# Optimization experiments

Hardware: AMD Instinct MI355X
Metric: run time of the kernel (lower is better)

Reference implementation:

```python
import jax, jax.numpy as jnp
import numpy as np

B, S, D, H = 8, 1024, 1024, 32


def setup_inputs() -> dict:
    key = jax.random.key(0)
    ks = jax.random.split(key, 32)
    w = lambda k, shape: jax.random.normal(k, shape, jnp.float32) * 0.02
    inp = {
        "poi_emb": jax.random.normal(ks[0], (B, S, D), jnp.float32),
        "svi_emb": jax.random.normal(ks[1], (B, S, D), jnp.float32),
        "poly_emb": jax.random.normal(ks[2], (B, S, D), jnp.float32),
        # shared multi-head attention (one module reused for all 4 calls)
        "Wq": w(ks[3], (D, D)), "bq": w(ks[4], (D,)),
        "Wk": w(ks[5], (D, D)), "bk": w(ks[6], (D,)),
        "Wv": w(ks[7], (D, D)), "bv": w(ks[8], (D,)),
        "Wo": w(ks[9], (D, D)), "bo": w(ks[10], (D,)),
        # poi_trans / svi_trans / poly_trans: Linear -> ReLU -> LayerNorm
        "Wpoi": w(ks[11], (D, D)), "bpoi": w(ks[12], (D,)),
        "gpoi": jnp.ones((D,), jnp.float32), "betapoi": jnp.zeros((D,), jnp.float32),
        "Wsvi": w(ks[13], (D, D)), "bsvi": w(ks[14], (D,)),
        "gsvi": jnp.ones((D,), jnp.float32), "betasvi": jnp.zeros((D,), jnp.float32),
        "Wpoly": w(ks[15], (D, D)), "bpoly": w(ks[16], (D,)),
        "gpoly": jnp.ones((D,), jnp.float32), "betapoly": jnp.zeros((D,), jnp.float32),
        # gate (Linear(2D,D)+sigmoid), filtration_gate (Linear(2D,D)+relu), out_trans (Linear(D,D))
        "Wg": w(ks[17], (2 * D, D)), "bg": w(ks[18], (D,)),
        "Wf": w(ks[19], (2 * D, D)), "bf": w(ks[20], (D,)),
        "Wt": w(ks[21], (D, D)), "bt": w(ks[22], (D,)),
    }
    return inp


def _ln(x, g, b, eps=1e-5):
    m = x.mean(-1, keepdims=True)
    v = ((x - m) ** 2).mean(-1, keepdims=True)
    return (x - m) / jnp.sqrt(v + eps) * g + b


def _trans(x, W, b, g, be):
    return _ln(jax.nn.relu(x @ W + b), g, be)


def _mha(q, k, v, Wq, bq, Wk, bk, Wv, bv, Wo, bo):
    Bn, Sq, Dm = q.shape
    dk = Dm // H
    Q = (q @ Wq + bq).reshape(Bn, Sq, H, dk)
    K = (k @ Wk + bk).reshape(Bn, -1, H, dk)
    V = (v @ Wv + bv).reshape(Bn, -1, H, dk)
    scores = jnp.einsum('bqhd,bkhd->bhqk', Q, K) / jnp.sqrt(jnp.float32(dk))
    attn = jax.nn.softmax(scores, axis=-1)
    out = jnp.einsum('bhqk,bkhd->bqhd', attn, V).reshape(Bn, Sq, Dm)
    return out @ Wo + bo


def reference(poi_emb, svi_emb, poly_emb, Wq, bq, Wk, bk, Wv, bv, Wo, bo,
              Wpoi, bpoi, gpoi, betapoi, Wsvi, bsvi, gsvi, betasvi,
              Wpoly, bpoly, gpoly, betapoly, Wg, bg, Wf, bf, Wt, bt):
    mha = lambda q, k, v: _mha(q, k, v, Wq, bq, Wk, bk, Wv, bv, Wo, bo)

    poi = _trans(poi_emb, Wpoi, bpoi, gpoi, betapoi)
    svi = _trans(svi_emb, Wsvi, bsvi, gsvi, betasvi)
    svi_feat = mha(svi, poi, poi)
    poi_feat = mha(poi, svi_feat, svi_feat)
    poi_feat = poi_feat + poi
    svi_feat = svi_feat + svi
    gate = jax.nn.sigmoid(jnp.concatenate([poi_feat, svi_feat], -1) @ Wg + bg)
    svi_fusion = gate * poi_feat + (1.0 - gate) * svi_feat
    filt = jax.nn.relu(jnp.concatenate([poi_feat, svi_fusion], -1) @ Wf + bf)
    out = filt @ Wt + bt

    # num == 3 branch
    poly = _trans(poly_emb, Wpoly, bpoly, gpoly, betapoly)
    poi2 = out
    poly_feat = mha(poly, poi2, poi2)
    poi_feat2 = mha(poi2, poly_feat, poly_feat)
    poly_feat = poly_feat + poly
    poi_feat2 = poi_feat2 + poi2
    gate2 = jax.nn.sigmoid(jnp.concatenate([poi_feat2, poly_feat], -1) @ Wg + bg)
    poly_fusion = gate2 * poi_feat2 + (1.0 - gate2) * poly_feat
    filt2 = jax.nn.relu(jnp.concatenate([poi_feat2, poly_fusion], -1) @ Wf + bf)
    return filt2 @ Wt + bt
```

## Files before the change

### kernel.cpp

```cpp
#include <hip/hip_runtime.h>
#include <hip/hip_bf16.h>


typedef unsigned short u16;
typedef __bf16 bf16x8_t __attribute__((ext_vector_type(8)));
typedef float f32x4 __attribute__((ext_vector_type(4)));

__device__ __forceinline__ u16 f2bf(float f) {
  union { __hip_bfloat16 h; u16 u; } c; c.h = __float2bfloat16(f); return c.u;
}
__device__ __forceinline__ float bf2f(u16 u) {
  union { unsigned v; float f; } c; c.v = ((unsigned)u) << 16; return c.f;
}

__device__ __forceinline__ void gl16(const void* g, void* l) {
  __builtin_amdgcn_global_load_lds((const __attribute__((address_space(1))) unsigned*)g,
                                   (__attribute__((address_space(3))) unsigned*)l, 16, 0, 0);
}

__global__ void fill_kernel(float4* o, float v) {
  int i = blockIdx.x * 256 + threadIdx.x;
  float4 x = {v, v, v, v};
  o[i] = x;
}

struct Conv3 { const float4* s[3]; ushort4* d[3]; };
__global__ void conv3_kernel(Conv3 p) {
  int seg = blockIdx.x >> 13;
  int i = (blockIdx.x & 8191) * 256 + threadIdx.x;
  float4 v = p.s[seg][i];
  ushort4 o; o.x = f2bf(v.x); o.y = f2bf(v.y); o.z = f2bf(v.z); o.w = f2bf(v.w);
  p.d[seg][i] = o;
}

struct WPack { const float* s[8]; u16* d[8]; };
__global__ void transpose_w_kernel(WPack p, int K) {
  const float* W = p.s[blockIdx.z];
  u16* Wt = p.d[blockIdx.z];
  __shared__ float tile[32][33];
  int tx = threadIdx.x, ty = threadIdx.y;
  int n0 = blockIdx.x * 32, k0 = blockIdx.y * 32;
#pragma unroll
  for (int i = 0; i < 4; i++)
    tile[ty + 8 * i][tx] = W[(size_t)(k0 + ty + 8 * i) * 1024 + n0 + tx];
  __syncthreads();
#pragma unroll
  for (int i = 0; i < 4; i++)
    Wt[(size_t)(n0 + ty + 8 * i) * K + k0 + tx] = f2bf(tile[tx][ty + 8 * i]);
}

struct GemmSeg {
  const u16 *A, *A2, *Bt;
  const float *bias, *bias1, *resF;
  float* outF; u16 *outH0, *outH1;
  const u16 *fx, *fy;
  int K, act, nctl, blk0;
  float oscale;
};
struct GemmArgs { GemmSeg s[3]; int nseg; int nwg8; };

__global__ __launch_bounds__(256) void gemm_mega(GemmArgs ga) {
  int orig = blockIdx.x;
  int bid = (orig & 7) * ga.nwg8 + (orig >> 3);
  int si = 0;
  if (ga.nseg > 1 && bid >= ga.s[1].blk0) si = 1;
  if (ga.nseg > 2 && bid >= ga.s[2].blk0) si = 2;
  GemmSeg sg = ga.s[si];
  int lb = bid - sg.blk0;
  int nct = 1 << sg.nctl;
  int bx = lb & (nct - 1), by = lb >> sg.nctl;

  __shared__ __align__(16) u16 lA[128 * 64];
  __shared__ __align__(16) u16 lB[128 * 64];
  int tid = threadIdx.x, lane = tid & 63, w = tid >> 6;
  int g = lane >> 4, li = lane & 15;
  int row0 = by * 128, col0 = bx * 128;
  int wr = (w >> 1) * 64, wc = (w & 1) * 64;
  f32x4 acc[4][4] = {};

  for (int k0 = 0; k0 < sg.K; k0 += 64) {
    const u16* Abase = (k0 < 1024) ? sg.A : sg.A2;
    int ka = k0 & 1023;
#pragma unroll
    for (int i = 0; i < 4; i++) {
      int c = tid + i * 256; int r = c >> 3, kc = c & 7;
      gl16(Abase + (size_t)(row0 + r) * 1024 + ka + kc * 8, lA + c * 8);
    }
#pragma unroll
    for (int i = 0; i < 4; i++) {
      int c = tid + i * 256; int n = c >> 3, kc = c & 7;
      gl16(sg.Bt + (size_t)(col0 + n) * sg.K + k0 + kc * 8, lB + c * 8);
    }
    __syncthreads();
#pragma unroll
    for (int kk = 0; kk < 2; kk++) {
      bf16x8_t af[4], bfr[4];
#pragma unroll
      for (int mr = 0; mr < 4; mr++)
        af[mr] = *(const bf16x8_t*)(lA + (wr + mr * 16 + li) * 64 + kk * 32 + g * 8);
#pragma unroll
      for (int nr = 0; nr < 4; nr++)
        bfr[nr] = *(const bf16x8_t*)(lB + (wc + nr * 16 + li) * 64 + kk * 32 + g * 8);
#pragma unroll
      for (int mr = 0; mr < 4; mr++)
#pragma unroll
        for (int nr = 0; nr < 4; nr++)
          acc[mr][nr] = __builtin_amdgcn_mfma_f32_16x16x32_bf16(af[mr], bfr[nr], acc[mr][nr], 0, 0, 0);
    }
    __syncthreads();
  }

#pragma unroll
  for (int nr = 0; nr < 4; nr++) {
    int col = col0 + wc + nr * 16 + li;
    int hi = col >> 10, colm = col & 1023;
    float bv = (hi ? sg.bias1 : sg.bias)[colm];
    u16* oh = hi ? sg.outH1 : sg.outH0;
#pragma unroll
    for (int mr = 0; mr < 4; mr++) {
      int rowb = row0 + wr + mr * 16 + g * 4;
#pragma unroll
      for (int r = 0; r < 4; r++) {
        size_t off = (size_t)(rowb + r) * 1024 + colm;
        float v = acc[mr][nr][r] + bv;
        if (sg.resF) v += sg.resF[off];
        if (sg.act == 1) v = fmaxf(v, 0.f);
        else if (sg.act == 2) {
          v = 1.f / (1.f + __expf(-v));
          if (sg.fx) v = v * bf2f(sg.fx[off]) + (1.f - v) * bf2f(sg.fy[off]);
        }
        v *= sg.oscale;
        if (sg.outF) sg.outF[off] = v;
        if (oh) oh[off] = f2bf(v);
      }
    }
  }
}

struct LnSeg { const u16* in; const float* ga; const float* be; float* outF; u16* outH; };
struct LnArgs { LnSeg s[3]; };
__global__ __launch_bounds__(256) void ln3_kernel(LnArgs la) {
  int seg = blockIdx.x >> 13;
  int row = blockIdx.x & 8191;
  LnSeg sg = la.s[seg];
  int t = threadIdx.x, lane = t & 63, w = t >> 6;
  ushort4 xi = ((const ushort4*)(sg.in + (size_t)row * 1024))[t];
  float4 x;
  x.x = fmaxf(bf2f(xi.x), 0.f); x.y = fmaxf(bf2f(xi.y), 0.f);
  x.z = fmaxf(bf2f(xi.z), 0.f); x.w = fmaxf(bf2f(xi.w), 0.f);
  float s1 = x.x + x.y + x.z + x.w;
  float s2 = x.x * x.x + x.y * x.y + x.z * x.z + x.w * x.w;
#pragma unroll
  for (int m = 1; m < 64; m <<= 1) { s1 += __shfl_xor(s1, m); s2 += __shfl_xor(s2, m); }
  __shared__ float red[8];
  if (lane == 0) { red[w] = s1; red[4 + w] = s2; }
  __syncthreads();
  s1 = red[0] + red[1] + red[2] + red[3];
  s2 = red[4] + red[5] + red[6] + red[7];
  float mean = s1 * (1.f / 1024.f);
  float var = s2 * (1.f / 1024.f) - mean * mean;
  float rstd = rsqrtf(var + 1e-5f);
  float4 gg = ((const float4*)sg.ga)[t], bb = ((const float4*)sg.be)[t];
  float4 y;
  y.x = (x.x - mean) * rstd * gg.x + bb.x;
  y.y = (x.y - mean) * rstd * gg.y + bb.y;
  y.z = (x.z - mean) * rstd * gg.z + bb.z;
  y.w = (x.w - mean) * rstd * gg.w + bb.w;
  if (sg.outF) ((float4*)(sg.outF + (size_t)row * 1024))[t] = y;
  ushort4 h; h.x = f2bf(y.x); h.y = f2bf(y.y); h.z = f2bf(y.z); h.w = f2bf(y.w);
  ((ushort4*)(sg.outH + (size_t)row * 1024))[t] = h;
}

__global__ void add2_kernel(const ushort4* __restrict__ a, const ushort4* __restrict__ b,
                            ushort4* __restrict__ o) {
  int i = blockIdx.x * 256 + threadIdx.x;
  ushort4 x = a[i], y = b[i];
  ushort4 h;
  h.x = f2bf(bf2f(x.x) + bf2f(y.x)); h.y = f2bf(bf2f(x.y) + bf2f(y.y));
  h.z = f2bf(bf2f(x.z) + bf2f(y.z)); h.w = f2bf(bf2f(x.w) + bf2f(y.w));
  o[i] = h;
}

__global__ __launch_bounds__(256) void attn_kernel(
    const u16* __restrict__ Q, const u16* __restrict__ Kb,
    const u16* __restrict__ Vb, u16* __restrict__ O) {
  int orig = blockIdx.x;
  int bid = (orig & 7) * 512 + (orig >> 3);
  int qt = bid & 15, h = (bid >> 4) & 31, b = bid >> 9;
  int tid = threadIdx.x, lane = tid & 63, w = tid >> 6;
  int g = lane >> 4, li = lane & 15;
  __shared__ __align__(16) u16 lK[128 * 40];
  __shared__ __align__(16) u16 lV[32 * 152];
  __shared__ __align__(16) u16 lP[4][16 * 152];
  int q0 = qt * 64 + w * 16;

  bf16x8_t aq = *(const bf16x8_t*)(Q + ((size_t)(b * 1024 + q0 + li) << 10) + h * 32 + g * 8);
  const f32x4 fzero = {0.f, 0.f, 0.f, 0.f};
  f32x4 oacc[2] = {};
  float mrun[4], lrun[4];
#pragma unroll
  for (int r = 0; r < 4; r++) { mrun[r] = -1e30f; lrun[r] = 0.f; }

  for (int kt = 0; kt < 1024; kt += 128) {
    __syncthreads();
#pragma unroll
    for (int i = 0; i < 2; i++) {
      int c2 = tid + i * 256; int key = c2 >> 2, ch = c2 & 3;
      uint4 v = *(const uint4*)(Kb + ((size_t)(b * 1024 + kt + key) << 10) + h * 32 + ch * 8);
      *(uint4*)(lK + key * 40 + ch * 8) = v;
    }
    {
      int p = tid >> 2, ch = tid & 3;
      const u16* vb0 = Vb + ((size_t)(b * 1024 + kt + 2 * p) << 10) + h * 32 + ch * 8;
      uint4 a = *(const uint4*)(vb0);
      uint4 bb = *(const uint4*)(vb0 + 1024);
      unsigned* lv32 = (unsigned*)lV;
#pragma unroll
      for (int j = 0; j < 4; j++) {
        unsigned ax = ((const unsigned*)&a)[j], bx = ((const unsigned*)&bb)[j];
        lv32[(8 * ch + 2 * j) * 76 + p]     = (ax & 0xffffu) | (bx << 16);
        lv32[(8 * ch + 2 * j + 1) * 76 + p] = (ax >> 16) | (bx & 0xffff0000u);
      }
    }
    __syncthreads();

    f32x4 s[8];
#pragma unroll
    for (int sub = 0; sub < 8; sub++) {
      bf16x8_t bk = *(const bf16x8_t*)(lK + (sub * 16 + li) * 40 + g * 8);
      s[sub] = __builtin_amdgcn_mfma_f32_16x16x32_bf16(aq, bk, fzero, 0, 0, 0);
    }
    float mx[4];
#pragma unroll
    for (int r = 0; r < 4; r++) mx[r] = -1e30f;
#pragma unroll
    for (int sub = 0; sub < 8; sub++)
#pragma unroll
      for (int r = 0; r < 4; r++) mx[r] = fmaxf(mx[r], s[sub][r]);
#pragma unroll
    for (int m = 1; m < 16; m <<= 1)
#pragma unroll
      for (int r = 0; r < 4; r++) mx[r] = fmaxf(mx[r], __shfl_xor(mx[r], m));
    bool keep = (mx[0] <= mrun[0] + 8.f) && (mx[1] <= mrun[1] + 8.f) &&
                (mx[2] <= mrun[2] + 8.f) && (mx[3] <= mrun[3] + 8.f);
    if (!__all(keep)) {
#pragma unroll
      for (int r = 0; r < 4; r++) {
        float mn = fmaxf(mrun[r], mx[r]);
        float corr = exp2f(mrun[r] - mn);
        mrun[r] = mn; lrun[r] *= corr;
        oacc[0][r] *= corr; oacc[1][r] *= corr;
      }
    }
    float rs[4] = {0.f, 0.f, 0.f, 0.f};
#pragma unroll
    for (int sub = 0; sub < 8; sub++)
#pragma unroll
      for (int r = 0; r < 4; r++) {
        float p = exp2f(s[sub][r] - mrun[r]);
        s[sub][r] = p; rs[r] += p;
      }
#pragma unroll
    for (int m = 1; m < 16; m <<= 1)
#pragma unroll
      for (int r = 0; r < 4; r++) rs[r] += __shfl_xor(rs[r], m);
#pragma unroll
    for (int r = 0; r < 4; r++) lrun[r] += rs[r];
#pragma unroll
    for (int sub = 0; sub < 8; sub++)
#pragma unroll
      for (int r = 0; r < 4; r++)
        lP[w][(g * 4 + r) * 152 + sub * 16 + li] = f2bf(s[sub][r]);
#pragma unroll
    for (int ks = 0; ks < 4; ks++) {
      bf16x8_t ap = *(const bf16x8_t*)(lP[w] + li * 152 + ks * 32 + g * 8);
#pragma unroll
      for (int nt = 0; nt < 2; nt++) {
        bf16x8_t bv = *(const bf16x8_t*)(lV + (nt * 16 + li) * 152 + ks * 32 + g * 8);
        oacc[nt] = __builtin_amdgcn_mfma_f32_16x16x32_bf16(ap, bv, oacc[nt], 0, 0, 0);
      }
    }
  }
#pragma unroll
  for (int r = 0; r < 4; r++) {
    float inv = 1.f / lrun[r];
#pragma unroll
    for (int nt = 0; nt < 2; nt++)
      O[((size_t)(b * 1024 + q0 + g * 4 + r) << 10) + h * 32 + nt * 16 + li] =
          f2bf(oacc[nt][r] * inv);
  }
}

static GemmSeg mk(const u16* A, const u16* A2, const u16* Bt,
                  const float* bias, const float* bias1, const float* resF,
                  float* outF, u16* oh0, u16* oh1, const u16* fx, const u16* fy,
                  int K, int act, int nctl, float osc) {
  GemmSeg s; s.A = A; s.A2 = A2; s.Bt = Bt; s.bias = bias; s.bias1 = bias1;
  s.resF = resF; s.outF = outF; s.outH0 = oh0; s.outH1 = oh1; s.fx = fx; s.fy = fy;
  s.K = K; s.act = act; s.nctl = nctl; s.blk0 = 0; s.oscale = osc;
  return s;
}

extern "C" void kernel_launch(void* const* d_in, const int* in_sizes, int n_in,
                              void* d_out, int out_size, void* d_ws, size_t ws_size,
                              hipStream_t stream) {
  const float* poi_emb = (const float*)d_in[0];
  const float* svi_emb = (const float*)d_in[1];
  const float* poly_emb = (const float*)d_in[2];
  const float *Wq = (const float*)d_in[3], *bq = (const float*)d_in[4];
  const float *Wk = (const float*)d_in[5], *bk = (const float*)d_in[6];
  const float *Wv = (const float*)d_in[7], *bv = (const float*)d_in[8];
  const float *Wo = (const float*)d_in[9], *bo = (const float*)d_in[10];
  const float *Wpoi = (const float*)d_in[11], *bpoi = (const float*)d_in[12];
  const float *gpoi = (const float*)d_in[13], *betapoi = (const float*)d_in[14];
  const float *Wsvi = (const float*)d_in[15], *bsvi = (const float*)d_in[16];
  const float *gsvi = (const float*)d_in[17], *betasvi = (const float*)d_in[18];
  const float *Wpoly = (const float*)d_in[19], *bpoly = (const float*)d_in[20];
  const float *gpoly = (const float*)d_in[21], *betapoly = (const float*)d_in[22];
  const float *Wg = (const float*)d_in[23], *bg = (const float*)d_in[24];
  const float *Wf = (const float*)d_in[25], *bfilt = (const float*)d_in[26];
  const float *Wt = (const float*)d_in[27], *bt = (const float*)d_in[28];

  const size_t MB = 1u << 20;
  if (ws_size < 168 * MB) {
    fill_kernel<<<out_size / 1024, 256, 0, stream>>>((float4*)d_out, 1e4f);
    return;
  }
  char* ws = (char*)d_ws;
  u16* WqT = (u16*)(ws + 0 * MB);    u16* WkT = (u16*)(ws + 2 * MB);
  u16* WvT = (u16*)(ws + 4 * MB);    u16* WoT = (u16*)(ws + 6 * MB);
  u16* WpoiT = (u16*)(ws + 8 * MB);  u16* WsviT = (u16*)(ws + 10 * MB);
  u16* WpolyT = (u16*)(ws + 12 * MB); u16* WtT = (u16*)(ws + 14 * MB);
  u16* WgT = (u16*)(ws + 16 * MB);   u16* WfT = (u16*)(ws + 20 * MB);
  u16* S0 = (u16*)(ws + 24 * MB);  u16* S1 = (u16*)(ws + 40 * MB);
  u16* S2 = (u16*)(ws + 56 * MB);  u16* S3 = (u16*)(ws + 72 * MB);
  u16* S4 = (u16*)(ws + 88 * MB);  u16* S5 = (u16*)(ws + 104 * MB);
  u16* S6 = (u16*)(ws + 120 * MB);
  float* F = (float*)(ws + 136 * MB);

  const float QS = 0.25503489f;

  WPack p8;
  p8.s[0]=Wq; p8.s[1]=Wk; p8.s[2]=Wv; p8.s[3]=Wo; p8.s[4]=Wpoi; p8.s[5]=Wsvi; p8.s[6]=Wpoly; p8.s[7]=Wt;
  p8.d[0]=WqT; p8.d[1]=WkT; p8.d[2]=WvT; p8.d[3]=WoT; p8.d[4]=WpoiT; p8.d[5]=WsviT; p8.d[6]=WpolyT; p8.d[7]=WtT;
  transpose_w_kernel<<<dim3(32, 32, 8), dim3(32, 8), 0, stream>>>(p8, 1024);
  WPack p2;
  p2.s[0]=Wg; p2.s[1]=Wf; p2.d[0]=WgT; p2.d[1]=WfT;
  for (int i = 2; i < 8; i++) { p2.s[i] = Wg; p2.d[i] = WgT; }
  transpose_w_kernel<<<dim3(32, 64, 2), dim3(32, 8), 0, stream>>>(p2, 2048);

  auto run1 = [&](GemmSeg a) {
    GemmArgs ga; ga.s[0] = a; ga.s[0].blk0 = 0; ga.nseg = 1;
    int nb = 64 << a.nctl; ga.nwg8 = nb / 8;
    gemm_mega<<<nb, 256, 0, stream>>>(ga);
  };
  auto run2 = [&](GemmSeg a, GemmSeg b) {
    GemmArgs ga; ga.s[0] = a; ga.s[1] = b;
    ga.s[0].blk0 = 0; ga.s[1].blk0 = 64 << a.nctl; ga.nseg = 2;
    int nb = (64 << a.nctl) + (64 << b.nctl); ga.nwg8 = nb / 8;
    gemm_mega<<<nb, 256, 0, stream>>>(ga);
  };
  auto run3 = [&](GemmSeg a, GemmSeg b, GemmSeg c) {
    GemmArgs ga; ga.s[0] = a; ga.s[1] = b; ga.s[2] = c;
    ga.s[0].blk0 = 0; ga.s[1].blk0 = 64 << a.nctl;
    ga.s[2].blk0 = ga.s[1].blk0 + (64 << b.nctl); ga.nseg = 3;
    int nb = ga.s[2].blk0 + (64 << c.nctl); ga.nwg8 = nb / 8;
    gemm_mega<<<nb, 256, 0, stream>>>(ga);
  };
  auto attn = [&](const u16* q, const u16* k, const u16* v, u16* o) {
    attn_kernel<<<4096, 256, 0, stream>>>(q, k, v, o);
  };
  auto add2 = [&](const u16* a, const u16* b, u16* o) {
    add2_kernel<<<8192, 256, 0, stream>>>((const ushort4*)a, (const ushort4*)b, (ushort4*)o);
  };

  Conv3 c3;
  c3.s[0] = (const float4*)poi_emb; c3.d[0] = (ushort4*)S0;
  c3.s[1] = (const float4*)svi_emb; c3.d[1] = (ushort4*)S1;
  c3.s[2] = (const float4*)poly_emb; c3.d[2] = (ushort4*)S2;
  conv3_kernel<<<24576, 256, 0, stream>>>(c3);

  run3(mk(S0, 0, WpoiT, bpoi, 0, 0, 0, S3, 0, 0, 0, 1024, 0, 3, 1.f),
       mk(S1, 0, WsviT, bsvi, 0, 0, 0, S4, 0, 0, 0, 1024, 0, 3, 1.f),
       mk(S2, 0, WpolyT, bpoly, 0, 0, 0, S5, 0, 0, 0, 1024, 0, 3, 1.f));
  LnArgs la;
  la.s[0] = LnSeg{S3, gpoi, betapoi, F, S3};
  la.s[1] = LnSeg{S4, gsvi, betasvi, 0, S4};
  la.s[2] = LnSeg{S5, gpoly, betapoly, 0, S5};
  ln3_kernel<<<24576, 256, 0, stream>>>(la);

  run2(mk(S4, 0, WqT, bq, 0, 0, 0, S0, 0, 0, 0, 1024, 0, 3, QS),
       mk(S3, 0, WkT, bk, bv, 0, 0, S1, S2, 0, 0, 1024, 0, 4, 1.f));
  attn(S0, S1, S2, S6);
  run2(mk(S6, 0, WoT, bo, 0, 0, 0, S0, 0, 0, 0, 1024, 0, 3, 1.f),
       mk(S3, 0, WqT, bq, 0, 0, 0, S1, 0, 0, 0, 1024, 0, 3, QS));
  run1(mk(S0, 0, WkT, bk, bv, 0, 0, S2, S6, 0, 0, 1024, 0, 4, 1.f));
  attn(S1, S2, S6, S3);
  run1(mk(S3, 0, WoT, bo, 0, F, 0, S1, 0, 0, 0, 1024, 0, 3, 1.f));
  add2(S0, S4, S4);
  run1(mk(S1, S4, WgT, bg, 0, 0, 0, S0, 0, S1, S4, 2048, 2, 3, 1.f));
  run1(mk(S1, S0, WfT, bfilt, 0, 0, 0, S2, 0, 0, 0, 2048, 1, 3, 1.f));
  run1(mk(S2, 0, WtT, bt, 0, 0, F, S6, 0, 0, 0, 1024, 0, 3, 1.f));

  run2(mk(S5, 0, WqT, bq, 0, 0, 0, S0, 0, 0, 0, 1024, 0, 3, QS),
       mk(S6, 0, WkT, bk, bv, 0, 0, S1, S2, 0, 0, 1024, 0, 4, 1.f));
  attn(S0, S1, S2, S3);
  run2(mk(S3, 0, WoT, bo, 0, 0, 0, S0, 0, 0, 0, 1024, 0, 3, 1.f),
       mk(S6, 0, WqT, bq, 0, 0, 0, S1, 0, 0, 0, 1024, 0, 3, QS));
  run1(mk(S0, 0, WkT, bk, bv, 0, 0, S2, S3, 0, 0, 1024, 0, 4, 1.f));
  attn(S1, S2, S3, S4);
  run1(mk(S4, 0, WoT, bo, 0, F, 0, S1, 0, 0, 0, 1024, 0, 3, 1.f));
  add2(S0, S5, S5);
  run1(mk(S1, S5, WgT, bg, 0, 0, 0, S0, 0, S1, S5, 2048, 2, 3, 1.f));
  run1(mk(S1, S0, WfT, bfilt, 0, 0, 0, S2, 0, 0, 0, 2048, 1, 3, 1.f));
  run1(mk(S2, 0, WtT, bt, 0, 0, (float*)d_out, 0, 0, 0, 0, 1024, 0, 3, 1.f));
}
```

Baseline: 1.825 ms.

## Restructure attention with register K loads, double-buffered V, MFMA row sums; add 64-row GEMM tiles

```diff
diff --git a/kernel.cpp b/kernel.cpp
--- a/kernel.cpp
+++ b/kernel.cpp
@@ -59,7 +59,9 @@
 };
 struct GemmArgs { GemmSeg s[3]; int nseg; int nwg8; };
 
+template <int BM>
 __global__ __launch_bounds__(256) void gemm_mega(GemmArgs ga) {
+  constexpr int MR = BM / 32;
   int orig = blockIdx.x;
   int bid = (orig & 7) * ga.nwg8 + (orig >> 3);
   int si = 0;
@@ -70,19 +72,19 @@
   int nct = 1 << sg.nctl;
   int bx = lb & (nct - 1), by = lb >> sg.nctl;
 
-  __shared__ __align__(16) u16 lA[128 * 64];
+  __shared__ __align__(16) u16 lA[BM * 64];
   __shared__ __align__(16) u16 lB[128 * 64];
   int tid = threadIdx.x, lane = tid & 63, w = tid >> 6;
   int g = lane >> 4, li = lane & 15;
-  int row0 = by * 128, col0 = bx * 128;
-  int wr = (w >> 1) * 64, wc = (w & 1) * 64;
-  f32x4 acc[4][4] = {};
+  int row0 = by * BM, col0 = bx * 128;
+  int wr = (w >> 1) * (BM / 2), wc = (w & 1) * 64;
+  f32x4 acc[MR][4] = {};
 
   for (int k0 = 0; k0 < sg.K; k0 += 64) {
     const u16* Abase = (k0 < 1024) ? sg.A : sg.A2;
     int ka = k0 & 1023;
 #pragma unroll
-    for (int i = 0; i < 4; i++) {
+    for (int i = 0; i < MR; i++) {
       int c = tid + i * 256; int r = c >> 3, kc = c & 7;
       gl16(Abase + (size_t)(row0 + r) * 1024 + ka + kc * 8, lA + c * 8);
     }
@@ -94,15 +96,15 @@
     __syncthreads();
 #pragma unroll
     for (int kk = 0; kk < 2; kk++) {
-      bf16x8_t af[4], bfr[4];
-#pragma unroll
-      for (int mr = 0; mr < 4; mr++)
+      bf16x8_t af[MR], bfr[4];
+#pragma unroll
+      for (int mr = 0; mr < MR; mr++)
         af[mr] = *(const bf16x8_t*)(lA + (wr + mr * 16 + li) * 64 + kk * 32 + g * 8);
 #pragma unroll
       for (int nr = 0; nr < 4; nr++)
         bfr[nr] = *(const bf16x8_t*)(lB + (wc + nr * 16 + li) * 64 + kk * 32 + g * 8);
 #pragma unroll
-      for (int mr = 0; mr < 4; mr++)
+      for (int mr = 0; mr < MR; mr++)
 #pragma unroll
         for (int nr = 0; nr < 4; nr++)
           acc[mr][nr] = __builtin_amdgcn_mfma_f32_16x16x32_bf16(af[mr], bfr[nr], acc[mr][nr], 0, 0, 0);
@@ -117,7 +119,7 @@
     float bv = (hi ? sg.bias1 : sg.bias)[colm];
     u16* oh = hi ? sg.outH1 : sg.outH0;
 #pragma unroll
-    for (int mr = 0; mr < 4; mr++) {
+    for (int mr = 0; mr < MR; mr++) {
       int rowb = row0 + wr + mr * 16 + g * 4;
 #pragma unroll
       for (int r = 0; r < 4; r++) {
@@ -189,101 +191,119 @@
   int qt = bid & 15, h = (bid >> 4) & 31, b = bid >> 9;
   int tid = threadIdx.x, lane = tid & 63, w = tid >> 6;
   int g = lane >> 4, li = lane & 15;
-  __shared__ __align__(16) u16 lK[128 * 40];
-  __shared__ __align__(16) u16 lV[32 * 152];
-  __shared__ __align__(16) u16 lP[4][16 * 152];
+  __shared__ __align__(16) u16 lV[(2 * 32 + 16) * 136];
+  __shared__ __align__(16) u16 lP[4][16 * 136];
   int q0 = qt * 64 + w * 16;
 
+  for (int i = tid; i < 16 * 136; i += 256) {
+    int rr = i / 136;
+    lV[8704 + i] = (rr == 0) ? (u16)0x3f80 : (u16)0;
+  }
+
   bf16x8_t aq = *(const bf16x8_t*)(Q + ((size_t)(b * 1024 + q0 + li) << 10) + h * 32 + g * 8);
+  const u16* kbase = Kb + ((size_t)(b * 1024 + li) << 10) + h * 32 + g * 8;
+  const u16* vb0 = Vb + ((size_t)(b * 1024 + 2 * lane) << 10) + h * 32 + w * 8;
+
   const f32x4 fzero = {0.f, 0.f, 0.f, 0.f};
-  f32x4 oacc[2] = {};
-  float mrun[4], lrun[4];
-#pragma unroll
-  for (int r = 0; r < 4; r++) { mrun[r] = -1e30f; lrun[r] = 0.f; }
-
-  for (int kt = 0; kt < 1024; kt += 128) {
-    __syncthreads();
-#pragma unroll
-    for (int i = 0; i < 2; i++) {
-      int c2 = tid + i * 256; int key = c2 >> 2, ch = c2 & 3;
-      uint4 v = *(const uint4*)(Kb + ((size_t)(b * 1024 + kt + key) << 10) + h * 32 + ch * 8);
-      *(uint4*)(lK + key * 40 + ch * 8) = v;
-    }
-    {
-      int p = tid >> 2, ch = tid & 3;
-      const u16* vb0 = Vb + ((size_t)(b * 1024 + kt + 2 * p) << 10) + h * 32 + ch * 8;
-      uint4 a = *(const uint4*)(vb0);
-      uint4 bb = *(const uint4*)(vb0 + 1024);
-      unsigned* lv32 = (unsigned*)lV;
+  f32x4 oacc[2] = {}; f32x4 osum = {};
+  float mrun[4];
+#pragma unroll
+  for (int r = 0; r < 4; r++) mrun[r] = -1e30f;
+
+  uint4 va, vb;
+  {
+    uint4 a0 = *(const uint4*)(vb0);
+    uint4 b0 = *(const uint4*)(vb0 + 1024);
+    unsigned* lv32 = (unsigned*)lV;
+#pragma unroll
+    for (int j = 0; j < 4; j++) {
+      unsigned ax = ((const unsigned*)&a0)[j], bx = ((const unsigned*)&b0)[j];
+      lv32[(8 * w + 2 * j) * 68 + lane]     = (ax & 0xffffu) | (bx << 16);
+      lv32[(8 * w + 2 * j + 1) * 68 + lane] = (ax >> 16) | (bx & 0xffff0000u);
+    }
+    va = *(const uint4*)(vb0 + ((size_t)1 << 17));
+    vb = *(const uint4*)(vb0 + ((size_t)1 << 17) + 1024);
+  }
+  __syncthreads();
+
+  for (int t = 0; t < 8; ++t) {
+    int kt = t << 7;
+    if (t) __syncthreads();
+    bf16x8_t kf[8];
+#pragma unroll
+    for (int sub = 0; sub < 8; sub++)
+      kf[sub] = *(const bf16x8_t*)(kbase + ((size_t)(kt + sub * 16) << 10));
+    if (t < 7) {
+      unsigned* lv32 = (unsigned*)(lV + ((t + 1) & 1) * 4352);
 #pragma unroll
       for (int j = 0; j < 4; j++) {
-        unsigned ax = ((const unsigned*)&a)[j], bx = ((const unsigned*)&bb)[j];
-        lv32[(8 * ch + 2 * j) * 76 + p]     = (ax & 0xffffu) | (bx << 16);
-        lv32[(8 * ch + 2 * j + 1) * 76 + p] = (ax >> 16) | (bx & 0xffff0000u);
+        unsigned ax = ((const unsigned*)&va)[j], bx = ((const unsigned*)&vb)[j];
+        lv32[(8 * w + 2 * j) * 68 + lane]     = (ax & 0xffffu) | (bx << 16);
+        lv32[(8 * w + 2 * j + 1) * 68 + lane] = (ax >> 16) | (bx & 0xffff0000u);
       }
-    }
-    __syncthreads();
+      if (t < 6) {
+        const u16* vn = vb0 + ((size_t)(t + 2) << 17);
+        va = *(const uint4*)(vn);
+        vb = *(const uint4*)(vn + 1024);
+      }
+    }
+    const u16* lVc = lV + (t & 1) * 4352;
 
     f32x4 s[8];
-#pragma unroll
-    for (int sub = 0; sub < 8; sub++) {
-      bf16x8_t bk = *(const bf16x8_t*)(lK + (sub * 16 + li) * 40 + g * 8);
-      s[sub] = __builtin_amdgcn_mfma_f32_16x16x32_bf16(aq, bk, fzero, 0, 0, 0);
-    }
-    float mx[4];
-#pragma unroll
-    for (int r = 0; r < 4; r++) mx[r] = -1e30f;
+    __builtin_amdgcn_s_setprio(1);
 #pragma unroll
     for (int sub = 0; sub < 8; sub++)
-#pragma unroll
-      for (int r = 0; r < 4; r++) mx[r] = fmaxf(mx[r], s[sub][r]);
-#pragma unroll
-    for (int m = 1; m < 16; m <<= 1)
-#pragma unroll
-      for (int r = 0; r < 4; r++) mx[r] = fmaxf(mx[r], __shfl_xor(mx[r], m));
-    bool keep = (mx[0] <= mrun[0] + 8.f) && (mx[1] <= mrun[1] + 8.f) &&
-                (mx[2] <= mrun[2] + 8.f) && (mx[3] <= mrun[3] + 8.f);
+      s[sub] = __builtin_amdgcn_mfma_f32_16x16x32_bf16(aq, kf[sub], fzero, 0, 0, 0);
+    __builtin_amdgcn_s_setprio(0);
+
+    float mxl[4];
+#pragma unroll
+    for (int r = 0; r < 4; r++) mxl[r] = s[0][r];
+#pragma unroll
+    for (int sub = 1; sub < 8; sub++)
+#pragma unroll
+      for (int r = 0; r < 4; r++) mxl[r] = fmaxf(mxl[r], s[sub][r]);
+    bool keep = (mxl[0] <= mrun[0] + 8.f) && (mxl[1] <= mrun[1] + 8.f) &&
+                (mxl[2] <= mrun[2] + 8.f) && (mxl[3] <= mrun[3] + 8.f);
     if (!__all(keep)) {
+      float mx[4] = {mxl[0], mxl[1], mxl[2], mxl[3]};
+#pragma unroll
+      for (int m = 1; m < 16; m <<= 1)
+#pragma unroll
+        for (int r = 0; r < 4; r++) mx[r] = fmaxf(mx[r], __shfl_xor(mx[r], m));
 #pragma unroll
       for (int r = 0; r < 4; r++) {
         float mn = fmaxf(mrun[r], mx[r]);
         float corr = exp2f(mrun[r] - mn);
-        mrun[r] = mn; lrun[r] *= corr;
-        oacc[0][r] *= corr; oacc[1][r] *= corr;
+        mrun[r] = mn;
+        oacc[0][r] *= corr; oacc[1][r] *= corr; osum[r] *= corr;
       }
     }
-    float rs[4] = {0.f, 0.f, 0.f, 0.f};
 #pragma unroll
     for (int sub = 0; sub < 8; sub++)
 #pragma unroll
-      for (int r = 0; r < 4; r++) {
-        float p = exp2f(s[sub][r] - mrun[r]);
-        s[sub][r] = p; rs[r] += p;
+      for (int r = 0; r < 4; r++)
+        lP[w][(g * 4 + r) * 136 + sub * 16 + li] = f2bf(exp2f(s[sub][r] - mrun[r]));
+    __builtin_amdgcn_s_setprio(1);
+#pragma unroll
+    for (int ks = 0; ks < 4; ks++) {
+      bf16x8_t ap = *(const bf16x8_t*)(lP[w] + li * 136 + ks * 32 + g * 8);
+#pragma unroll
+      for (int nt = 0; nt < 2; nt++) {
+        bf16x8_t bv2 = *(const bf16x8_t*)(lVc + (nt * 16 + li) * 136 + ks * 32 + g * 8);
+        oacc[nt] = __builtin_amdgcn_mfma_f32_16x16x32_bf16(ap, bv2, oacc[nt], 0, 0, 0);
       }
-#pragma unroll
-    for (int m = 1; m < 16; m <<= 1)
-#pragma unroll
-      for (int r = 0; r < 4; r++) rs[r] += __shfl_xor(rs[r], m);
-#pragma unroll
-    for (int r = 0; r < 4; r++) lrun[r] += rs[r];
-#pragma unroll
-    for (int sub = 0; sub < 8; sub++)
-#pragma unroll
-      for (int r = 0; r < 4; r++)
-        lP[w][(g * 4 + r) * 152 + sub * 16 + li] = f2bf(s[sub][r]);
-#pragma unroll
-    for (int ks = 0; ks < 4; ks++) {
-      bf16x8_t ap = *(const bf16x8_t*)(lP[w] + li * 152 + ks * 32 + g * 8);
-#pragma unroll
-      for (int nt = 0; nt < 2; nt++) {
-        bf16x8_t bv = *(const bf16x8_t*)(lV + (nt * 16 + li) * 152 + ks * 32 + g * 8);
-        oacc[nt] = __builtin_amdgcn_mfma_f32_16x16x32_bf16(ap, bv, oacc[nt], 0, 0, 0);
-      }
-    }
-  }
+      bf16x8_t bvs = *(const bf16x8_t*)(lV + 8704 + li * 136 + ks * 32 + g * 8);
+      osum = __builtin_amdgcn_mfma_f32_16x16x32_bf16(ap, bvs, osum, 0, 0, 0);
+    }
+    __builtin_amdgcn_s_setprio(0);
+  }
+  float lr[4];
+#pragma unroll
+  for (int r = 0; r < 4; r++) lr[r] = __shfl(osum[r], lane & 48);
 #pragma unroll
   for (int r = 0; r < 4; r++) {
-    float inv = 1.f / lrun[r];
+    float inv = 1.f / lr[r];
 #pragma unroll
     for (int nt = 0; nt < 2; nt++)
       O[((size_t)(b * 1024 + q0 + g * 4 + r) << 10) + h * 32 + nt * 16 + li] =
@@ -352,20 +372,25 @@
   auto run1 = [&](GemmSeg a) {
     GemmArgs ga; ga.s[0] = a; ga.s[0].blk0 = 0; ga.nseg = 1;
     int nb = 64 << a.nctl; ga.nwg8 = nb / 8;
-    gemm_mega<<<nb, 256, 0, stream>>>(ga);
+    gemm_mega<128><<<nb, 256, 0, stream>>>(ga);
+  };
+  auto run1_64 = [&](GemmSeg a) {
+    GemmArgs ga; ga.s[0] = a; ga.s[0].blk0 = 0; ga.nseg = 1;
+    int nb = 128 << a.nctl; ga.nwg8 = nb / 8;
+    gemm_mega<64><<<nb, 256, 0, stream>>>(ga);
   };
   auto run2 = [&](GemmSeg a, GemmSeg b) {
     GemmArgs ga; ga.s[0] = a; ga.s[1] = b;
     ga.s[0].blk0 = 0; ga.s[1].blk0 = 64 << a.nctl; ga.nseg = 2;
     int nb = (64 << a.nctl) + (64 << b.nctl); ga.nwg8 = nb / 8;
-    gemm_mega<<<nb, 256, 0, stream>>>(ga);
+    gemm_mega<128><<<nb, 256, 0, stream>>>(ga);
   };
   auto run3 = [&](GemmSeg a, GemmSeg b, GemmSeg c) {
     GemmArgs ga; ga.s[0] = a; ga.s[1] = b; ga.s[2] = c;
     ga.s[0].blk0 = 0; ga.s[1].blk0 = 64 << a.nctl;
     ga.s[2].blk0 = ga.s[1].blk0 + (64 << b.nctl); ga.nseg = 3;
     int nb = ga.s[2].blk0 + (64 << c.nctl); ga.nwg8 = nb / 8;
-    gemm_mega<<<nb, 256, 0, stream>>>(ga);
+    gemm_mega<128><<<nb, 256, 0, stream>>>(ga);
   };
   auto attn = [&](const u16* q, const u16* k, const u16* v, u16* o) {
     attn_kernel<<<4096, 256, 0, stream>>>(q, k, v, o);
@@ -396,11 +421,11 @@
        mk(S3, 0, WqT, bq, 0, 0, 0, S1, 0, 0, 0, 1024, 0, 3, QS));
   run1(mk(S0, 0, WkT, bk, bv, 0, 0, S2, S6, 0, 0, 1024, 0, 4, 1.f));
   attn(S1, S2, S6, S3);
-  run1(mk(S3, 0, WoT, bo, 0, F, 0, S1, 0, 0, 0, 1024, 0, 3, 1.f));
+  run1_64(mk(S3, 0, WoT, bo, 0, F, 0, S1, 0, 0, 0, 1024, 0, 3, 1.f));
   add2(S0, S4, S4);
-  run1(mk(S1, S4, WgT, bg, 0, 0, 0, S0, 0, S1, S4, 2048, 2, 3, 1.f));
-  run1(mk(S1, S0, WfT, bfilt, 0, 0, 0, S2, 0, 0, 0, 2048, 1, 3, 1.f));
-  run1(mk(S2, 0, WtT, bt, 0, 0, F, S6, 0, 0, 0, 1024, 0, 3, 1.f));
+  run1_64(mk(S1, S4, WgT, bg, 0, 0, 0, S0, 0, S1, S4, 2048, 2, 3, 1.f));
+  run1_64(mk(S1, S0, WfT, bfilt, 0, 0, 0, S2, 0, 0, 0, 2048, 1, 3, 1.f));
+  run1_64(mk(S2, 0, WtT, bt, 0, 0, F, S6, 0, 0, 0, 1024, 0, 3, 1.f));
 
   run2(mk(S5, 0, WqT, bq, 0, 0, 0, S0, 0, 0, 0, 1024, 0, 3, QS),
        mk(S6, 0, WkT, bk, bv, 0, 0, S1, S2, 0, 0, 1024, 0, 4, 1.f));
@@ -409,9 +434,9 @@
        mk(S6, 0, WqT, bq, 0, 0, 0, S1, 0, 0, 0, 1024, 0, 3, QS));
   run1(mk(S0, 0, WkT, bk, bv, 0, 0, S2, S3, 0, 0, 1024, 0, 4, 1.f));
   attn(S1, S2, S3, S4);
-  run1(mk(S4, 0, WoT, bo, 0, F, 0, S1, 0, 0, 0, 1024, 0, 3, 1.f));
+  run1_64(mk(S4, 0, WoT, bo, 0, F, 0, S1, 0, 0, 0, 1024, 0, 3, 1.f));
   add2(S0, S5, S5);
-  run1(mk(S1, S5, WgT, bg, 0, 0, 0, S0, 0, S1, S5, 2048, 2, 3, 1.f));
-  run1(mk(S1, S0, WfT, bfilt, 0, 0, 0, S2, 0, 0, 0, 2048, 1, 3, 1.f));
-  run1(mk(S2, 0, WtT, bt, 0, 0, (float*)d_out, 0, 0, 0, 0, 1024, 0, 3, 1.f));
-}
+  run1_64(mk(S1, S5, WgT, bg, 0, 0, 0, S0, 0, S1, S5, 2048, 2, 3, 1.f));
+  run1_64(mk(S1, S0, WfT, bfilt, 0, 0, 0, S2, 0, 0, 0, 2048, 1, 3, 1.f));
+  run1_64(mk(S2, 0, WtT, bt, 0, 0, (float*)d_out, 0, 0, 0, 0, 1024, 0, 3, 1.f));
+}
```

New measurement: 1.815 ms. Within noise of the previous version (-0.6%).
